# Kernel tuning notes

Measured on AMD Instinct MI355X. Metric: run time of the kernel, lower is better.

Reference implementation:

```python
import jax, jax.numpy as jnp
import numpy as np

N_NODES = 70000
N_EDGES = 2_000_000
IN_CH, FEAT_CH, OUT_CH = 1044, 128, 3


def _gcn_norm(src_sl, dst_sl, n_nodes, dtype):
    # PyG gcn_norm with add_self_loops=True, edge_weight=1:
    # deg over target nodes, norm = deg^-1/2[src] * deg^-1/2[dst]
    deg = jax.ops.segment_sum(jnp.ones(src_sl.shape[0], dtype=dtype), dst_sl,
                              num_segments=n_nodes)
    dinv = jnp.where(deg > 0, jax.lax.rsqrt(deg), jnp.zeros((), dtype))
    return dinv[src_sl] * dinv[dst_sl]


def _gcn_layer(x, src_sl, dst_sl, norm, W, b, n_nodes):
    h = x @ W                                  # [N, out] linear transform first
    msg = h[src_sl] * norm[:, None]            # gather + scale
    out = jax.ops.segment_sum(msg, dst_sl, num_segments=n_nodes)  # scatter-add
    return out + b


def setup_inputs() -> dict:
    key = jax.random.key(0)
    ks = jax.random.split(key, 6)
    features = jax.random.normal(ks[0], (N_NODES, IN_CH), dtype=jnp.float32)
    edges = jax.random.randint(ks[1], (2, N_EDGES), 0, N_NODES, dtype=jnp.int64)
    edges2 = jax.random.randint(ks[2], (2, N_EDGES), 0, N_NODES, dtype=jnp.int64)
    edge_features = jax.random.normal(ks[3], (N_EDGES,), dtype=jnp.float32)
    W1 = jax.random.normal(ks[4], (IN_CH, FEAT_CH), dtype=jnp.float32) * (1.0 / np.sqrt(IN_CH))
    b1 = jnp.zeros((FEAT_CH,), dtype=jnp.float32)
    W2 = jax.random.normal(ks[5], (FEAT_CH, OUT_CH), dtype=jnp.float32) * (1.0 / np.sqrt(FEAT_CH))
    b2 = jnp.zeros((OUT_CH,), dtype=jnp.float32)
    return {"features": features, "edges": edges, "edges2": edges2,
            "edge_features": edge_features, "W1": W1, "b1": b1, "W2": W2, "b2": b2}


def reference(features, edges, edges2, edge_features, W1, b1, W2, b2):
    # edge_features is discarded by the module (set to None); edges2 unused.
    n = features.shape[0]
    loop = jnp.arange(n, dtype=edges.dtype)
    src_sl = jnp.concatenate([edges[0], loop])  # self-loops appended
    dst_sl = jnp.concatenate([edges[1], loop])
    norm = _gcn_norm(src_sl, dst_sl, n, features.dtype)
    x = _gcn_layer(features, src_sl, dst_sl, norm, W1, b1, n)
    x = jax.nn.relu(x)
    # dropout is identity in eval mode (deterministic reference)
    return _gcn_layer(x, src_sl, dst_sl, norm, W2, b2, n)
```

## Files before the change

### kernel.cpp

```cpp
#include <hip/hip_runtime.h>
#include <hip/hip_bf16.h>

#define K_IN   1044
#define N_FEAT 128
#define KPAD   1056
#define NSTEP  (KPAD / 32)
#define BM     96

#define NB     512
#define BWMAX  256
#define EPB    8192

typedef __attribute__((ext_vector_type(8))) short short8;
typedef __attribute__((ext_vector_type(4))) float f32x4;

__device__ __forceinline__ ushort f2bf(float f) {
  unsigned x = __float_as_uint(f);
  x += 0x7fffu + ((x >> 16) & 1u);
  return (ushort)(x >> 16);
}
__device__ __forceinline__ uint pkbf(float lo, float hi) {
  __hip_bfloat162 h = __float22bfloat162_rn(make_float2(lo, hi));
  return *reinterpret_cast<uint*>(&h);
}
__device__ __forceinline__ float bflo(uint v) { return __uint_as_float(v << 16); }
__device__ __forceinline__ float bfhi(uint v) { return __uint_as_float(v & 0xFFFF0000u); }

__device__ __forceinline__ void gld16(const void* g, void* l) {
  __builtin_amdgcn_global_load_lds(
      (const __attribute__((address_space(1))) unsigned int*)g,
      (__attribute__((address_space(3))) unsigned int*)l, 16, 0, 0);
}


__global__ __launch_bounds__(256) void csr_hist_kernel(const int* __restrict__ dst,
                                                       int* __restrict__ bt, int E, int bw) {
  __shared__ int h[NB];
  const int t = threadIdx.x;
  for (int i = t; i < NB; i += 256) h[i] = 0;
  __syncthreads();
  const int e0 = blockIdx.x * EPB;
  const int e1 = min(e0 + EPB, E);
  for (int e = e0 + t; e < e1; e += 256) atomicAdd(&h[dst[e] / bw], 1);
  __syncthreads();
  for (int i = t; i < NB; i += 256)
    if (h[i]) atomicAdd(&bt[i], h[i]);
}

__global__ __launch_bounds__(256) void csr_bucket_scan_kernel(const int* __restrict__ bt,
                                                              int* __restrict__ bucket_base,
                                                              int* __restrict__ bucket_cursor) {
  __shared__ int sc[256];
  const int t = threadIdx.x;
  int v0 = bt[2 * t], v1 = bt[2 * t + 1];
  int s = v0 + v1;
  sc[t] = s;
  __syncthreads();
  for (int off = 1; off < 256; off <<= 1) {
    int x = (t >= off) ? sc[t - off] : 0;
    __syncthreads();
    sc[t] += x;
    __syncthreads();
  }
  int excl = sc[t] - s;
  bucket_base[2 * t]     = excl;
  bucket_base[2 * t + 1] = excl + v0;
  bucket_cursor[2 * t]     = excl;
  bucket_cursor[2 * t + 1] = excl + v0;
  if (t == 255) bucket_base[NB] = sc[255];
}

__global__ __launch_bounds__(256) void csr_stage_kernel(const int* __restrict__ src,
                                                        const int* __restrict__ dst,
                                                        int* __restrict__ bucket_cursor,
                                                        uint* __restrict__ staging, int E, int bw) {
  __shared__ int h[NB];
  __shared__ int cur[NB];
  const int t = threadIdx.x;
  for (int i = t; i < NB; i += 256) h[i] = 0;
  __syncthreads();
  const int e0 = blockIdx.x * EPB;
  const int e1 = min(e0 + EPB, E);
  for (int e = e0 + t; e < e1; e += 256) atomicAdd(&h[dst[e] / bw], 1);
  __syncthreads();
  for (int i = t; i < NB; i += 256)
    cur[i] = h[i] ? atomicAdd(&bucket_cursor[i], h[i]) : 0;
  __syncthreads();
  for (int e = e0 + t; e < e1; e += 256) {
    int d = dst[e];
    int b = d / bw;
    int p = atomicAdd(&cur[b], 1);
    staging[p] = ((uint)src[e] << 8) | (uint)(d - b * bw);
  }
}

__global__ __launch_bounds__(256) void csr_final_kernel(const uint* __restrict__ staging,
                                                        const int* __restrict__ bucket_base,
                                                        int* __restrict__ row_ptr,
                                                        int* __restrict__ sorted_src,
                                                        float* __restrict__ dinv,
                                                        int N, int bw, int E) {
  __shared__ int hist[BWMAX];
  __shared__ int sc[256];
  const int b = blockIdx.x;
  const int t = threadIdx.x;
  if (b == 0 && t == 0) row_ptr[N] = E;
  const int node0 = b * bw;
  const int nn = min(bw, N - node0);
  if (nn <= 0) return;
  const int base = bucket_base[b];
  const int cnt  = bucket_base[b + 1] - base;

  for (int i = t; i < BWMAX; i += 256) hist[i] = 0;
  __syncthreads();
  for (int i = t; i < cnt; i += 256)
    atomicAdd(&hist[staging[base + i] & 255u], 1);
  __syncthreads();
  int v = (t < nn) ? hist[t] : 0;
  if (t < nn) dinv[node0 + t] = rsqrtf((float)(v + 1));
  sc[t] = v;
  __syncthreads();
  for (int off = 1; off < 256; off <<= 1) {
    int x = (t >= off) ? sc[t - off] : 0;
    __syncthreads();
    sc[t] += x;
    __syncthreads();
  }
  int excl = sc[t] - v;
  if (t < nn) row_ptr[node0 + t] = base + excl;
  if (t < nn) hist[t] = excl;
  __syncthreads();
  for (int i = t; i < cnt; i += 256) {
    uint p = staging[base + i];
    int c = atomicAdd(&hist[p & 255u], 1);
    sorted_src[base + c] = (int)(p >> 8);
  }
}


__global__ void convert_w1_kernel(const float* __restrict__ W1, ushort* __restrict__ W1T) {
  int idx = blockIdx.x * blockDim.x + threadIdx.x;
  if (idx >= N_FEAT * KPAD) return;
  int col = idx / KPAD, k = idx - col * KPAD;
  int kk = k & ~31;
  int jp = (k >> 3) & 3;
  int e  = k & 7;
  int jl = jp ^ (col & 3);
  int ksrc = kk + 8 * jl + e;
  W1T[idx] = (ksrc < K_IN) ? f2bf(W1[(size_t)ksrc * N_FEAT + col]) : (ushort)0;
}


__global__ __launch_bounds__(256) void gemm1_mfma_kernel(const float* __restrict__ X,
                                                         const ushort* __restrict__ W1T,
                                                         const float* __restrict__ dinv,
                                                         ushort* __restrict__ G1, int M) {
  __shared__ float  Af[2][BM * 32];
  __shared__ ushort Bsb[2][128 * 32];

  const int t = threadIdx.x;
  const int row0 = blockIdx.x * BM;
  const int w = t >> 6, l = t & 63;
  const int w24 = w * 24, w32 = w * 32;
  const int Mm1 = M - 1;

  const int wm = w >> 1, wn = w & 1;
  const int lr = l & 15, g = l >> 4;
  const int k7 = lr & 7, k3 = lr & 3;

  f32x4 acc[3][4] = {};

  auto stage = [&](int s, int buf) {
    const int kk = s * 32;
    #pragma unroll
    for (int i = 0; i < 3; i++) {
      int r  = w24 + i * 8 + (l >> 3);
      int jl = (l & 7) ^ (r & 7);
      int grow = min(row0 + r, Mm1);
      int gk   = min(kk + 4 * jl, K_IN - 4);
      gld16(X + (size_t)grow * K_IN + gk, (void*)&Af[buf][(w24 + i * 8) * 32]);
    }
    #pragma unroll
    for (int i = 0; i < 2; i++) {
      int r = w32 + i * 16 + (l >> 2);
      gld16(W1T + (size_t)r * KPAD + kk + 8 * (l & 3),
            (void*)&Bsb[buf][(w32 + i * 16) * 32]);
    }
  };

  stage(0, 0);
  __syncthreads();

  int cur = 0;
  #pragma unroll 1
  for (int s = 0; s < NSTEP; s++) {
    if (s + 1 < NSTEP) stage(s + 1, cur ^ 1);

    short8 af[3], bfr[4];
    #pragma unroll
    for (int m = 0; m < 3; m++) {
      const float* rp = &Af[cur][(wm * 48 + m * 16 + lr) * 32];
      float4 a0 = *(const float4*)&rp[((2 * g + 0) ^ k7) << 2];
      float4 a1 = *(const float4*)&rp[((2 * g + 1) ^ k7) << 2];
      uint4 uu = make_uint4(pkbf(a0.x, a0.y), pkbf(a0.z, a0.w),
                            pkbf(a1.x, a1.y), pkbf(a1.z, a1.w));
      af[m] = *(short8*)&uu;
    }
    #pragma unroll
    for (int n = 0; n < 4; n++)
      bfr[n] = *(const short8*)&Bsb[cur][(wn * 64 + n * 16 + lr) * 32 + ((g ^ k3) << 3)];

    #pragma unroll
    for (int m = 0; m < 3; m++)
      #pragma unroll
      for (int n = 0; n < 4; n++)
        acc[m][n] = __builtin_amdgcn_mfma_f32_16x16x32_bf16(af[m], bfr[n], acc[m][n], 0, 0, 0);

    __syncthreads();
    cur ^= 1;
  }

  const int rbase = row0 + wm * 48 + (l >> 4) * 4;
  const int cbase = wn * 64 + lr;
  #pragma unroll
  for (int m = 0; m < 3; m++) {
    #pragma unroll
    for (int r = 0; r < 4; r++) {
      int row = rbase + m * 16 + r;
      if (row < M) {
        float dv = dinv[row];
        #pragma unroll
        for (int n = 0; n < 4; n++)
          G1[(size_t)row * N_FEAT + cbase + n * 16] = f2bf(dv * acc[m][n][r]);
      }
    }
  }
}


__global__ __launch_bounds__(256) void agg1mm_kernel(const ushort* __restrict__ G1,
                                                     const int* __restrict__ row_ptr,
                                                     const int* __restrict__ sorted_src,
                                                     const float* __restrict__ dinv,
                                                     const float* __restrict__ b1,
                                                     const float* __restrict__ W2,
                                                     float* __restrict__ G2, int N) {
  const int w = (blockIdx.x * blockDim.x + threadIdx.x) >> 6;
  const int lane = threadIdx.x & 63;
  if (w >= N) return;
  const int beg = row_ptr[w], end = row_ptr[w + 1];
  const uint* g1u = (const uint*)G1;
  const int co = lane;

  uint vs = g1u[((size_t)w << 6) + co];
  float a0 = bflo(vs), a1 = bfhi(vs);

  int e = beg;
  for (; e + 8 <= end; e += 8) {
    int s[8];
    #pragma unroll
    for (int i = 0; i < 8; i++) s[i] = sorted_src[e + i];
    #pragma unroll
    for (int i = 0; i < 8; i++) {
      uint v = g1u[((size_t)s[i] << 6) + co];
      a0 += bflo(v); a1 += bfhi(v);
    }
  }
  for (; e < end; e++) {
    uint v = g1u[((size_t)sorted_src[e] << 6) + co];
    a0 += bflo(v); a1 += bfhi(v);
  }

  const float di = dinv[w];
  float r0 = fmaxf(fmaf(di, a0, b1[2 * co + 0]), 0.f);
  float r1 = fmaxf(fmaf(di, a1, b1[2 * co + 1]), 0.f);

  const float* wrow = W2 + 6 * co;
  float s0 = r0 * wrow[0] + r1 * wrow[3];
  float s1 = r0 * wrow[1] + r1 * wrow[4];
  float s2 = r0 * wrow[2] + r1 * wrow[5];
  #pragma unroll
  for (int off = 32; off > 0; off >>= 1) {
    s0 += __shfl_down(s0, off);
    s1 += __shfl_down(s1, off);
    s2 += __shfl_down(s2, off);
  }
  if (lane == 0) {
    G2[w * 3 + 0] = di * s0;
    G2[w * 3 + 1] = di * s1;
    G2[w * 3 + 2] = di * s2;
  }
}


__global__ __launch_bounds__(256) void agg2_kernel(const float* __restrict__ G2,
                                                   const int* __restrict__ row_ptr,
                                                   const int* __restrict__ sorted_src,
                                                   const float* __restrict__ dinv,
                                                   const float* __restrict__ b2,
                                                   float* __restrict__ out, int N) {
  int t = blockIdx.x * blockDim.x + threadIdx.x;
  int node = t >> 6, lane = t & 63;
  if (node >= N) return;
  int beg = row_ptr[node], end = row_ptr[node + 1];
  float a0 = 0.f, a1 = 0.f, a2 = 0.f;
  for (int e = beg + lane; e < end; e += 64) {
    int s = sorted_src[e];
    a0 += G2[s * 3 + 0];
    a1 += G2[s * 3 + 1];
    a2 += G2[s * 3 + 2];
  }
  #pragma unroll
  for (int off = 32; off > 0; off >>= 1) {
    a0 += __shfl_down(a0, off);
    a1 += __shfl_down(a1, off);
    a2 += __shfl_down(a2, off);
  }
  if (lane == 0) {
    float di = dinv[node];
    out[node * 3 + 0] = di * (a0 + G2[node * 3 + 0]) + b2[0];
    out[node * 3 + 1] = di * (a1 + G2[node * 3 + 1]) + b2[1];
    out[node * 3 + 2] = di * (a2 + G2[node * 3 + 2]) + b2[2];
  }
}


extern "C" void kernel_launch(void* const* d_in, const int* in_sizes, int n_in,
                              void* d_out, int out_size, void* d_ws, size_t ws_size,
                              hipStream_t stream) {
  const float* features = (const float*)d_in[0];
  const int*   edges    = (const int*)d_in[1];
  const float* W1 = (const float*)d_in[4];
  const float* b1 = (const float*)d_in[5];
  const float* W2 = (const float*)d_in[6];
  const float* b2 = (const float*)d_in[7];
  float* out = (float*)d_out;

  const int N = in_sizes[0] / K_IN;
  const int E = in_sizes[1] / 2;
  const int* src = edges;
  const int* dst = edges + E;
  const int bw = (N + NB - 1) / NB;

  char* ws = (char*)d_ws;
  size_t off = 0;
  auto alloc = [&](size_t bytes) {
    void* p = ws + off;
    off += (bytes + 255) & ~(size_t)255;
    return p;
  };
  int*    bt            = (int*)   alloc((size_t)NB * sizeof(int));
  int*    bucket_base   = (int*)   alloc((size_t)(NB + 1) * sizeof(int));
  int*    bucket_cursor = (int*)   alloc((size_t)NB * sizeof(int));
  int*    row_ptr       = (int*)   alloc((size_t)(N + 1) * sizeof(int));
  float*  dinv          = (float*) alloc((size_t)N * sizeof(float));
  uint*   staging       = (uint*)  alloc((size_t)E * sizeof(uint));
  int*    sorted_src    = (int*)   alloc((size_t)E * sizeof(int));
  ushort* G1            = (ushort*)alloc((size_t)N * N_FEAT * sizeof(ushort));
  float*  G2            = (float*) alloc((size_t)N * 3 * sizeof(float));
  ushort* W1T           = (ushort*)alloc((size_t)N_FEAT * KPAD * sizeof(ushort));
  (void)ws_size;

  const int eblocks = (E + EPB - 1) / EPB;

  hipMemsetAsync(bt, 0, (size_t)NB * sizeof(int), stream);
  convert_w1_kernel<<<(N_FEAT * KPAD + 255) / 256, 256, 0, stream>>>(W1, W1T);
  csr_hist_kernel<<<eblocks, 256, 0, stream>>>(dst, bt, E, bw);
  csr_bucket_scan_kernel<<<1, 256, 0, stream>>>(bt, bucket_base, bucket_cursor);
  csr_stage_kernel<<<eblocks, 256, 0, stream>>>(src, dst, bucket_cursor, staging, E, bw);
  csr_final_kernel<<<NB, 256, 0, stream>>>(staging, bucket_base, row_ptr, sorted_src, dinv, N, bw, E);
  gemm1_mfma_kernel<<<(N + BM - 1) / BM, 256, 0, stream>>>(features, W1T, dinv, G1, N);
  agg1mm_kernel<<<((size_t)N * 64 + 255) / 256, 256, 0, stream>>>(G1, row_ptr, sorted_src, dinv, b1, W2, G2, N);
  agg2_kernel<<<((size_t)N * 64 + 255) / 256, 256, 0, stream>>>(G2, row_ptr, sorted_src, dinv, b2, out, N);
}
```

Baseline: 259.8 us.

## Triple-buffer GEMM A tiles with vmcnt waits and pad G2 to float4

The GEMM1 kernel now prefetches the fp32 feature tile two steps ahead using three LDS buffers, while B stays double-buffered. The full __syncthreads is replaced by explicit s_waitcnt vmcnt plus s_barrier, so only the oldest loads are waited on. This hides more global-load latency in the bandwidth-bound X read, at the cost of extra LDS, which may lower occupancy. Separately, G2 is padded to 4 floats per node so agg2 gathers with one 16-byte load instead of three scalar loads.

```diff
diff --git a/kernel.cpp b/kernel.cpp
--- a/kernel.cpp
+++ b/kernel.cpp
@@ -155,7 +155,7 @@
                                                          const ushort* __restrict__ W1T,
                                                          const float* __restrict__ dinv,
                                                          ushort* __restrict__ G1, int M) {
-  __shared__ float  Af[2][BM * 32];
+  __shared__ float  Af[3][BM * 32];
   __shared__ ushort Bsb[2][128 * 32];
 
   const int t = threadIdx.x;
@@ -170,7 +170,7 @@
 
   f32x4 acc[3][4] = {};
 
-  auto stage = [&](int s, int buf) {
+  auto stage_A = [&](int s, int buf) {
     const int kk = s * 32;
     #pragma unroll
     for (int i = 0; i < 3; i++) {
@@ -180,6 +180,9 @@
       int gk   = min(kk + 4 * jl, K_IN - 4);
       gld16(X + (size_t)grow * K_IN + gk, (void*)&Af[buf][(w24 + i * 8) * 32]);
     }
+  };
+  auto stage_B = [&](int s, int buf) {
+    const int kk = s * 32;
     #pragma unroll
     for (int i = 0; i < 2; i++) {
       int r = w32 + i * 16 + (l >> 2);
@@ -188,18 +191,23 @@
     }
   };
 
-  stage(0, 0);
-  __syncthreads();
-
-  int cur = 0;
+  stage_A(0, 0);
+  stage_B(0, 0);
+  stage_A(1, 1);
+  asm volatile("s_waitcnt vmcnt(3)" ::: "memory");
+  __builtin_amdgcn_sched_barrier(0);
+  __builtin_amdgcn_s_barrier();
+
   #pragma unroll 1
   for (int s = 0; s < NSTEP; s++) {
-    if (s + 1 < NSTEP) stage(s + 1, cur ^ 1);
+    const int ab = s % 3, bb = s & 1;
+    if (s + 1 < NSTEP) stage_B(s + 1, (s + 1) & 1);
+    if (s + 2 < NSTEP) stage_A(s + 2, (s + 2) % 3);
 
     short8 af[3], bfr[4];
     #pragma unroll
     for (int m = 0; m < 3; m++) {
-      const float* rp = &Af[cur][(wm * 48 + m * 16 + lr) * 32];
+      const float* rp = &Af[ab][(wm * 48 + m * 16 + lr) * 32];
       float4 a0 = *(const float4*)&rp[((2 * g + 0) ^ k7) << 2];
       float4 a1 = *(const float4*)&rp[((2 * g + 1) ^ k7) << 2];
       uint4 uu = make_uint4(pkbf(a0.x, a0.y), pkbf(a0.z, a0.w),
@@ -208,7 +216,7 @@
     }
     #pragma unroll
     for (int n = 0; n < 4; n++)
-      bfr[n] = *(const short8*)&Bsb[cur][(wn * 64 + n * 16 + lr) * 32 + ((g ^ k3) << 3)];
+      bfr[n] = *(const short8*)&Bsb[bb][(wn * 64 + n * 16 + lr) * 32 + ((g ^ k3) << 3)];
 
     #pragma unroll
     for (int m = 0; m < 3; m++)
@@ -216,8 +224,10 @@
       for (int n = 0; n < 4; n++)
         acc[m][n] = __builtin_amdgcn_mfma_f32_16x16x32_bf16(af[m], bfr[n], acc[m][n], 0, 0, 0);
 
-    __syncthreads();
-    cur ^= 1;
+    if (s + 2 < NSTEP) { asm volatile("s_waitcnt vmcnt(3)" ::: "memory"); }
+    else               { asm volatile("s_waitcnt vmcnt(0)" ::: "memory"); }
+    __builtin_amdgcn_sched_barrier(0);
+    __builtin_amdgcn_s_barrier();
   }
 
   const int rbase = row0 + wm * 48 + (l >> 4) * 4;
@@ -286,9 +296,7 @@
     s2 += __shfl_down(s2, off);
   }
   if (lane == 0) {
-    G2[w * 3 + 0] = di * s0;
-    G2[w * 3 + 1] = di * s1;
-    G2[w * 3 + 2] = di * s2;
+    *(float4*)&G2[(size_t)w * 4] = make_float4(di * s0, di * s1, di * s2, 0.f);
   }
 }
 
@@ -305,10 +313,8 @@
   int beg = row_ptr[node], end = row_ptr[node + 1];
   float a0 = 0.f, a1 = 0.f, a2 = 0.f;
   for (int e = beg + lane; e < end; e += 64) {
-    int s = sorted_src[e];
-    a0 += G2[s * 3 + 0];
-    a1 += G2[s * 3 + 1];
-    a2 += G2[s * 3 + 2];
+    float4 v = *(const float4*)&G2[(size_t)sorted_src[e] * 4];
+    a0 += v.x; a1 += v.y; a2 += v.z;
   }
   #pragma unroll
   for (int off = 32; off > 0; off >>= 1) {
@@ -318,9 +324,10 @@
   }
   if (lane == 0) {
     float di = dinv[node];
-    out[node * 3 + 0] = di * (a0 + G2[node * 3 + 0]) + b2[0];
-    out[node * 3 + 1] = di * (a1 + G2[node * 3 + 1]) + b2[1];
-    out[node * 3 + 2] = di * (a2 + G2[node * 3 + 2]) + b2[2];
+    float4 self = *(const float4*)&G2[(size_t)node * 4];
+    out[node * 3 + 0] = di * (a0 + self.x) + b2[0];
+    out[node * 3 + 1] = di * (a1 + self.y) + b2[1];
+    out[node * 3 + 2] = di * (a2 + self.z) + b2[2];
   }
 }
 
@@ -357,7 +364,7 @@
   uint*   staging       = (uint*)  alloc((size_t)E * sizeof(uint));
   int*    sorted_src    = (int*)   alloc((size_t)E * sizeof(int));
   ushort* G1            = (ushort*)alloc((size_t)N * N_FEAT * sizeof(ushort));
-  float*  G2            = (float*) alloc((size_t)N * 3 * sizeof(float));
+  float*  G2            = (float*) alloc((size_t)N * 4 * sizeof(float));
   ushort* W1T           = (ushort*)alloc((size_t)N_FEAT * KPAD * sizeof(ushort));
   (void)ws_size;
 
```

Measured after the change: 255.2 us. No clear change (-1.8%).
